# Performance work log

Measured on AMD Instinct MI355X. Metric: run time of the kernel, lower is better.

Reference implementation:

```python
import jax, jax.numpy as jnp
import numpy as np

DIM = 3072
HEADS = 24
HDIM = 128
MLP = 12288           # dim * mlp_ratio
B = 2
TEXT = 256
IMG = 1024
S = TEXT + IMG
TAU = 5.0
EPS = 1e-6


def setup_inputs() -> dict:
    key = jax.random.key(0)
    ks = jax.random.split(key, 16)
    w = lambda k, shape: jax.random.normal(k, shape, jnp.float32) * 0.02
    # rotary tables (cos/sin over pair dim HDIM//2)
    pos = jnp.arange(S, dtype=jnp.float32)
    inv_freq = 1.0 / (10000.0 ** (jnp.arange(0, HDIM, 2, dtype=jnp.float32) / HDIM))
    ang = pos[:, None] * inv_freq[None, :]            # [S, HDIM//2]
    return {
        "hidden_states": jax.random.normal(ks[0], (B, S, DIM), jnp.float32),
        "temb": jax.random.normal(ks[1], (B, DIM), jnp.float32),
        "rot_cos": jnp.cos(ang),
        "rot_sin": jnp.sin(ang),
        # AdaLayerNormZeroSingle: linear(silu(temb)) -> shift, scale, gate
        "w_ada": w(ks[2], (DIM, 3 * DIM)), "b_ada": jnp.zeros((3 * DIM,), jnp.float32),
        # attention qkv (bias=True) + rms_norm scales
        "wq": w(ks[3], (DIM, DIM)), "bq": jnp.zeros((DIM,), jnp.float32),
        "wk": w(ks[4], (DIM, DIM)), "bk": jnp.zeros((DIM,), jnp.float32),
        "wv": w(ks[5], (DIM, DIM)), "bv": jnp.zeros((DIM,), jnp.float32),
        "q_scale": jnp.ones((HDIM,), jnp.float32), "k_scale": jnp.ones((HDIM,), jnp.float32),
        # TokenSelect (conditioning proj + per-token score head)
        "w_cond": w(ks[6], (DIM, DIM)), "b_cond": jnp.zeros((DIM,), jnp.float32),
        "w_sel": w(ks[7], (DIM, 1)), "b_sel": jnp.zeros((1,), jnp.float32),
        # proj_mlp (DynaLinear, full width) and proj_out
        "w1": w(ks[8], (DIM, MLP)), "b1": jnp.zeros((MLP,), jnp.float32),
        "w2": w(ks[9], (DIM + MLP, DIM)), "b2": jnp.zeros((DIM,), jnp.float32),
        "text_len": TEXT,
        "img_len": IMG,
    }


def _forward(hidden_states, temb, rot_cos, rot_sin, w_ada, b_ada, wq, bq, wk, bk,
             wv, bv, q_scale, k_scale, w_cond, b_cond, w_sel, b_sel, w1, b1, w2, b2,
             text_len, img_len):
    Bn, Sn, C = hidden_states.shape
    residual = hidden_states

    # --- AdaLayerNormZeroSingle ---
    e = jax.nn.silu(temb) @ w_ada + b_ada
    shift, scale, gate = jnp.split(e, 3, axis=-1)          # each [B, C]
    mu = hidden_states.mean(-1, keepdims=True)
    var = hidden_states.var(-1, keepdims=True)
    x = (hidden_states - mu) * jax.lax.rsqrt(var + EPS)
    x = x * (1.0 + scale[:, None, :]) + shift[:, None, :]  # norm_hidden_states

    # --- self-attention (pre_only: no out proj), qk rms_norm, rope ---
    split_heads = lambda t: t.reshape(Bn, Sn, HEADS, HDIM)
    q = split_heads(x @ wq + bq)
    k = split_heads(x @ wk + bk)
    v = split_heads(x @ wv + bv)
    rmsn = lambda t, g: t * jax.lax.rsqrt(jnp.mean(t * t, -1, keepdims=True) + EPS) * g
    q = rmsn(q, q_scale)
    k = rmsn(k, k_scale)

    def rope(t):
        t1, t2 = t[..., 0::2], t[..., 1::2]
        c = rot_cos[None, :, None, :]
        s = rot_sin[None, :, None, :]
        r1 = t1 * c - t2 * s
        r2 = t1 * s + t2 * c
        return jnp.stack([r1, r2], axis=-1).reshape(t.shape)

    q, k = rope(q), rope(k)
    scores = jnp.einsum("bqhd,bkhd->bhqk", q, k) / np.float32(np.sqrt(HDIM))
    attn = jax.nn.softmax(scores, axis=-1)
    attn_out = jnp.einsum("bhqk,bkhd->bqhd", attn, v).reshape(Bn, Sn, C)

    # --- token selection on raw hidden states (img tokens, cond on temb + text) ---
    img_h = hidden_states[:, text_len:, :]
    text_h = hidden_states[:, :text_len, :]
    cond = jax.nn.silu(temb + text_h.mean(axis=1)) @ w_cond + b_cond   # [B, C]
    logits = (img_h + cond[:, None, :]) @ w_sel + b_sel                # [B, IMG, 1]
    soft = jax.nn.sigmoid(logits / TAU)
    hard = (soft > 0.5).astype(soft.dtype)
    mask = hard + soft - jax.lax.stop_gradient(soft)   # straight-through hard mask

    gelu = lambda t: jax.nn.gelu(t, approximate=True)

    # text branch: full-width dyna MLP
    text_mlp = gelu(x[:, :text_len] @ w1 + b1)
    text_out = jnp.concatenate([attn_out[:, :text_len], text_mlp], axis=-1) @ w2 + b2

    # img branch: gather/MLP/scatter is math-equivalent to masked dense compute
    # (unselected rows stay zero in the scatter buffer)
    img_mlp = gelu(x[:, text_len:] @ w1 + b1)
    img_out = (jnp.concatenate([attn_out[:, text_len:], img_mlp], axis=-1) @ w2 + b2) * mask

    out = jnp.concatenate([text_out, img_out], axis=1)
    return residual + gate[:, None, :] * out


def reference(hidden_states, temb, rot_cos, rot_sin, w_ada, b_ada, wq, bq, wk, bk,
              wv, bv, q_scale, k_scale, w_cond, b_cond, w_sel, b_sel, w1, b1, w2, b2,
              text_len, img_len):
    return _forward(hidden_states, temb, rot_cos, rot_sin, w_ada, b_ada, wq, bq, wk,
                    bk, wv, bv, q_scale, k_scale, w_cond, b_cond, w_sel, b_sel,
                    w1, b1, w2, b2, text_len, img_len)
```

## Files before the change

kernel.cpp:

```cpp
#include <hip/hip_runtime.h>
#include <hip/hip_bf16.h>


#define DIM    3072
#define NHEADS 24
#define HD     128
#define MLPD   12288
#define NB     2
#define TEXTL  256
#define IMGL   1024
#define SEQL   1280
#define NTOK   (NB*SEQL)
#define CATK   (DIM+MLPD)
#define EPSV   1e-6f

typedef unsigned short u16;
typedef __bf16 bf16x8 __attribute__((ext_vector_type(8)));
typedef float f32x4 __attribute__((ext_vector_type(4)));

__device__ __forceinline__ u16 f2bf(float f){
  unsigned u = __builtin_bit_cast(unsigned, f);
  u += 0x7fffu + ((u >> 16) & 1u);
  return (u16)(u >> 16);
}
__device__ __forceinline__ float siluf(float x){ return x / (1.f + __expf(-x)); }
__device__ __forceinline__ float geluf(float x){
  float t = 0.7978845608028654f * (x + 0.044715f * x * x * x);
  float th = 1.f - 2.f / (__expf(2.f * t) + 1.f);
  return 0.5f * x * (1.f + th);
}
__device__ __forceinline__ void ld_lds16(const void* g, void* l){
  __builtin_amdgcn_global_load_lds((const __attribute__((address_space(1))) void*)g,
                                   (__attribute__((address_space(3))) void*)l, 16, 0, 0);
}

__global__ __launch_bounds__(256)
void k_transpose_cvt(const float* __restrict__ W, u16* __restrict__ WT, int K, int N){
  __shared__ float tile[64][65];
  const int n0 = blockIdx.x * 64, k0 = blockIdx.y * 64;
  const int tx = threadIdx.x & 63, ty = threadIdx.x >> 6;
  #pragma unroll
  for (int i = 0; i < 16; ++i){
    const int r = ty + i*4;
    tile[r][tx] = W[(size_t)(k0 + r)*N + n0 + tx];
  }
  __syncthreads();
  #pragma unroll
  for (int i = 0; i < 16; ++i){
    const int r = ty + i*4;
    WT[(size_t)(n0 + r)*K + k0 + tx] = f2bf(tile[tx][r]);
  }
}

__global__ void k_cat3(const float* __restrict__ a, const float* __restrict__ b,
                       const float* __restrict__ c, float* __restrict__ o){
  const int i = blockIdx.x*256 + threadIdx.x;
  if (i < DIM) o[i] = a[i];
  else if (i < 2*DIM) o[i] = b[i - DIM];
  else o[i] = c[i - 2*DIM];
}

__global__ __launch_bounds__(256)
void k_ada(const float* __restrict__ temb, const float* __restrict__ w_ada,
           const float* __restrict__ b_ada, float* __restrict__ e){
  __shared__ float st[2*DIM];
  __shared__ float red[4][2][64];
  const int t = threadIdx.x;
  for (int i = t; i < 2*DIM; i += 256) st[i] = siluf(temb[i]);
  __syncthreads();
  const int tx = t & 63, ty = t >> 6;
  const int col = blockIdx.x*64 + tx;
  float a0 = 0.f, a1 = 0.f;
  for (int k = ty*768; k < ty*768 + 768; ++k){
    const float w = w_ada[(size_t)k*9216 + col];
    a0 += st[k]*w; a1 += st[DIM + k]*w;
  }
  red[ty][0][tx] = a0; red[ty][1][tx] = a1;
  __syncthreads();
  if (ty == 0){
    float s0 = red[0][0][tx] + red[1][0][tx] + red[2][0][tx] + red[3][0][tx];
    float s1 = red[0][1][tx] + red[1][1][tx] + red[2][1][tx] + red[3][1][tx];
    e[col]        = s0 + b_ada[col];
    e[9216 + col] = s1 + b_ada[col];
  }
}

__global__ void k_tmean(const float* __restrict__ h, float* __restrict__ tm){
  const int b = blockIdx.y;
  const int c = blockIdx.x*256 + threadIdx.x;
  float s = 0.f;
  for (int i = 0; i < TEXTL; ++i) s += h[((size_t)b*SEQL + i)*DIM + c];
  tm[b*DIM + c] = s * (1.f/TEXTL);
}

__global__ __launch_bounds__(256)
void k_cond(const float* __restrict__ temb, const float* __restrict__ tm,
            const float* __restrict__ w_cond, const float* __restrict__ b_cond,
            float* __restrict__ cond){
  __shared__ float st[2*DIM];
  __shared__ float red[4][2][64];
  const int t = threadIdx.x;
  for (int i = t; i < 2*DIM; i += 256) st[i] = siluf(temb[i] + tm[i]);
  __syncthreads();
  const int tx = t & 63, ty = t >> 6;
  const int col = blockIdx.x*64 + tx;
  float a0 = 0.f, a1 = 0.f;
  for (int k = ty*768; k < ty*768 + 768; ++k){
    const float w = w_cond[(size_t)k*DIM + col];
    a0 += st[k]*w; a1 += st[DIM + k]*w;
  }
  red[ty][0][tx] = a0; red[ty][1][tx] = a1;
  __syncthreads();
  if (ty == 0){
    float s0 = red[0][0][tx] + red[1][0][tx] + red[2][0][tx] + red[3][0][tx];
    float s1 = red[0][1][tx] + red[1][1][tx] + red[2][1][tx] + red[3][1][tx];
    cond[col]       = s0 + b_cond[col];
    cond[DIM + col] = s1 + b_cond[col];
  }
}

__global__ __launch_bounds__(256)
void k_sel(const float* __restrict__ h, const float* __restrict__ cond,
           const float* __restrict__ w_sel, const float* __restrict__ b_sel,
           float* __restrict__ maskb){
  const int lane = threadIdx.x & 63;
  const int wv = threadIdx.x >> 6;
  const int wid = blockIdx.x*4 + wv;
  const int b = wid >> 10, i = wid & 1023;
  const float* hr = h + ((size_t)b*SEQL + TEXTL + i)*DIM;
  const float* cr = cond + (size_t)b*DIM;
  float acc = 0.f;
  #pragma unroll
  for (int j = 0; j < 12; ++j){
    const int c4 = j*64 + lane;
    float4 hv = ((const float4*)hr)[c4];
    float4 cv = ((const float4*)cr)[c4];
    float4 wv4 = ((const float4*)w_sel)[c4];
    acc += (hv.x+cv.x)*wv4.x + (hv.y+cv.y)*wv4.y + (hv.z+cv.z)*wv4.z + (hv.w+cv.w)*wv4.w;
  }
  #pragma unroll
  for (int off = 1; off < 64; off <<= 1) acc += __shfl_xor(acc, off, 64);
  if (lane == 0) maskb[wid] = (acc + b_sel[0]) > 0.f ? 1.f : 0.f;
}

__global__ __launch_bounds__(256)
void k_lnmod(const float* __restrict__ h, const float* __restrict__ e,
             u16* __restrict__ xb){
  const int t = blockIdx.x;
  const int b = t / SEQL;
  const float* row = h + (size_t)t*DIM;
  float4 v[3];
  float s = 0.f, ss = 0.f;
  #pragma unroll
  for (int j = 0; j < 3; ++j){
    v[j] = ((const float4*)row)[threadIdx.x + j*256];
    s  += v[j].x + v[j].y + v[j].z + v[j].w;
    ss += v[j].x*v[j].x + v[j].y*v[j].y + v[j].z*v[j].z + v[j].w*v[j].w;
  }
  __shared__ float rs[4], rss[4];
  #pragma unroll
  for (int off = 1; off < 64; off <<= 1){
    s += __shfl_xor(s, off, 64); ss += __shfl_xor(ss, off, 64);
  }
  const int wv = threadIdx.x >> 6;
  if ((threadIdx.x & 63) == 0){ rs[wv] = s; rss[wv] = ss; }
  __syncthreads();
  s = rs[0]+rs[1]+rs[2]+rs[3]; ss = rss[0]+rss[1]+rss[2]+rss[3];
  const float mu = s * (1.f/DIM);
  const float var = ss * (1.f/DIM) - mu*mu;
  const float rstd = rsqrtf(var + EPSV);
  const float* sh = e + (size_t)b*9216;
  #pragma unroll
  for (int j = 0; j < 3; ++j){
    const int i4 = threadIdx.x + j*256;
    float4 sf = ((const float4*)sh)[i4];
    float4 sc = ((const float4*)(sh + DIM))[i4];
    ushort4 o;
    o.x = f2bf(((v[j].x - mu)*rstd)*(1.f + sc.x) + sf.x);
    o.y = f2bf(((v[j].y - mu)*rstd)*(1.f + sc.y) + sf.y);
    o.z = f2bf(((v[j].z - mu)*rstd)*(1.f + sc.z) + sf.z);
    o.w = f2bf(((v[j].w - mu)*rstd)*(1.f + sc.w) + sf.w);
    ((ushort4*)(xb + (size_t)t*DIM))[i4] = o;
  }
}

template<int MODE>
__global__ __launch_bounds__(256, 2)
void k_gemm(const u16* __restrict__ A, const u16* __restrict__ BT,
            const float* __restrict__ bias,
            float* __restrict__ Cf, u16* __restrict__ Cb,
            int K, int ldc, int col_off,
            size_t zsB, size_t zsC, size_t zsBias,
            const float* __restrict__ residual, const float* __restrict__ egate,
            const float* __restrict__ maskb){
  __shared__ __align__(16) u16 As[128*32];
  __shared__ __align__(16) u16 Bs[128*32];
  const int tid  = threadIdx.x;
  const int lane = tid & 63;
  const int wv   = tid >> 6;
  const int wr   = wv >> 1, wc = wv & 1;
  const int brow = blockIdx.y * 128, bcol = blockIdx.x * 128;
  const int l16 = lane & 15;
  const int g4  = lane >> 4;
  BT   += blockIdx.z * zsB;
  bias += blockIdx.z * zsBias;

  f32x4 acc[4][4] = {};
  const int nkt = K >> 5;
  for (int kt = 0; kt < nkt; ++kt){
    __syncthreads();
    #pragma unroll
    for (int c = 0; c < 2; ++c){
      const int Lb = wv*2048 + c*1024;
      const int row = (Lb + lane*16) >> 6;
      const int sch = (lane & 3) ^ ((row >> 1) & 3);
      ld_lds16(A + (size_t)(brow + row)*K + kt*32 + sch*8, (char*)As + Lb);
    }
    #pragma unroll
    for (int c = 0; c < 2; ++c){
      const int Lb = wv*2048 + c*1024;
      const int row = (Lb + lane*16) >> 6;
      const int sch = (lane & 3) ^ ((row >> 1) & 3);
      ld_lds16(BT + (size_t)(bcol + row)*K + kt*32 + sch*8, (char*)Bs + Lb);
    }
    __syncthreads();
    bf16x8 af[4], bfr[4];
    #pragma unroll
    for (int m = 0; m < 4; ++m){
      const int row = wr*64 + m*16 + l16;
      const int sch = g4 ^ ((row >> 1) & 3);
      af[m] = *(const bf16x8*)((const char*)As + row*64 + sch*16);
    }
    #pragma unroll
    for (int n = 0; n < 4; ++n){
      const int row = wc*64 + n*16 + l16;
      const int sch = g4 ^ ((row >> 1) & 3);
      bfr[n] = *(const bf16x8*)((const char*)Bs + row*64 + sch*16);
    }
    #pragma unroll
    for (int m = 0; m < 4; ++m)
      #pragma unroll
      for (int n = 0; n < 4; ++n)
        acc[m][n] = __builtin_amdgcn_mfma_f32_16x16x32_bf16(af[m], bfr[n], acc[m][n], 0, 0, 0);
  }
  float* Cfz = Cf + blockIdx.z * zsC;
  #pragma unroll
  for (int m = 0; m < 4; ++m){
    #pragma unroll
    for (int n = 0; n < 4; ++n){
      #pragma unroll
      for (int r = 0; r < 4; ++r){
        const int row = brow + wr*64 + m*16 + g4*4 + r;
        const int col = bcol + wc*64 + n*16 + l16;
        const float val = acc[m][n][r] + bias[col];
        if (MODE == 0){
          Cfz[(size_t)row*ldc + col] = val;
        } else if (MODE == 1){
          Cb[(size_t)row*ldc + col_off + col] = f2bf(geluf(val));
        } else {
          const int bb = row / SEQL;
          const int sidx = row - bb*SEQL;
          const float mk = (sidx < TEXTL) ? 1.f : maskb[bb*IMGL + sidx - TEXTL];
          Cfz[(size_t)row*ldc + col] = residual[(size_t)row*DIM + col]
                                     + egate[(size_t)bb*9216 + 2*DIM + col] * (val * mk);
        }
      }
    }
  }
}

__global__ __launch_bounds__(256)
void k_qkpost(const float* __restrict__ qkv, const float* __restrict__ rcos,
              const float* __restrict__ rsin, const float* __restrict__ qscale,
              const float* __restrict__ kscale, u16* __restrict__ qb,
              u16* __restrict__ kb){
  const int t = blockIdx.x;
  const int which = blockIdx.y;
  const float* src = qkv + ((size_t)which*NTOK + t)*DIM;
  const float* gvec = which == 0 ? qscale : kscale;
  u16* dst = which == 0 ? qb : kb;
  const int s = t % SEQL;
  const int lane = threadIdx.x & 63;
  const int wv = threadIdx.x >> 6;
  const int l32 = lane & 31;
  const int hh = lane >> 5;
  #pragma unroll
  for (int p = 0; p < 3; ++p){
    const int hidx = p*8 + wv*2 + hh;
    float4 v = ((const float4*)(src + hidx*HD))[l32];
    float ssq = v.x*v.x + v.y*v.y + v.z*v.z + v.w*v.w;
    #pragma unroll
    for (int off = 1; off < 32; off <<= 1) ssq += __shfl_xor(ssq, off, 64);
    const float rms = rsqrtf(ssq * (1.f/HD) + EPSV);
    const int d0 = l32*4;
    const float t0 = v.x*rms*gvec[d0],   t1 = v.y*rms*gvec[d0+1];
    const float t2 = v.z*rms*gvec[d0+2], t3 = v.w*rms*gvec[d0+3];
    const int i0 = l32*2;
    const float c0 = rcos[s*64 + i0],   s0 = rsin[s*64 + i0];
    const float c1 = rcos[s*64 + i0+1], s1 = rsin[s*64 + i0+1];
    ushort4 o;
    o.x = f2bf(t0*c0 - t1*s0);
    o.y = f2bf(t0*s0 + t1*c0);
    o.z = f2bf(t2*c1 - t3*s1);
    o.w = f2bf(t2*s1 + t3*c1);
    ((ushort4*)(dst + (size_t)t*DIM + hidx*HD))[l32] = o;
  }
}

__global__ __launch_bounds__(256)
void k_vpost(const float* __restrict__ qkv, u16* __restrict__ vt){
  __shared__ float tile[64][65];
  const int bh = blockIdx.x;
  const int st = blockIdx.y;
  const int dt = blockIdx.z;
  const int b = bh / NHEADS, hidx = bh % NHEADS;
  const float* v = qkv + (size_t)2*NTOK*DIM;
  const int tx = threadIdx.x & 63, ty = threadIdx.x >> 6;
  #pragma unroll
  for (int i = 0; i < 16; ++i){
    const int r = ty + i*4;
    tile[r][tx] = v[((size_t)b*SEQL + st*64 + r)*DIM + hidx*HD + dt*64 + tx];
  }
  __syncthreads();
  #pragma unroll
  for (int i = 0; i < 16; ++i){
    const int r = ty + i*4;
    vt[((size_t)bh*HD + dt*64 + r)*SEQL + st*64 + tx] = f2bf(tile[tx][r]);
  }
}

__global__ __launch_bounds__(256, 2)
void k_attn(const u16* __restrict__ q, const u16* __restrict__ kg,
            const u16* __restrict__ vt, u16* __restrict__ cat){
  __shared__ __align__(16) u16 Ks[64*128];
  __shared__ __align__(16) u16 Vs[128*64];
  __shared__ __align__(16) u16 Ps[4*16*64];
  const int lane = threadIdx.x & 63;
  const int wv = threadIdx.x >> 6;
  const int bh = blockIdx.y, b = bh / NHEADS, hidx = bh % NHEADS;
  const int qt = blockIdx.x;
  const int l16 = lane & 15;
  const int g4 = lane >> 4;

  bf16x8 qf[4];
  {
    const int qrow = qt*64 + wv*16 + l16;
    const u16* qptr = q + ((size_t)b*SEQL + qrow)*DIM + hidx*HD;
    #pragma unroll
    for (int ksi = 0; ksi < 4; ++ksi)
      qf[ksi] = *(const bf16x8*)(qptr + ksi*32 + g4*8);
  }
  f32x4 out[8] = {};
  float mreg[4] = {-1e30f, -1e30f, -1e30f, -1e30f};
  float lreg[4] = {0.f, 0.f, 0.f, 0.f};
  const float scl = 0.08838834764831845f;

  for (int kt = 0; kt < SEQL/64; ++kt){
    __syncthreads();
    #pragma unroll
    for (int c = 0; c < 4; ++c){
      const int Lb = wv*4096 + c*1024;
      const int row = (Lb + lane*16) >> 8;
      const int sch = (lane & 15) ^ (row & 7);
      ld_lds16(kg + ((size_t)b*SEQL + kt*64 + row)*DIM + hidx*HD + sch*8, (char*)Ks + Lb);
    }
    #pragma unroll
    for (int c = 0; c < 4; ++c){
      const int Lb = wv*4096 + c*1024;
      const int row = (Lb + lane*16) >> 7;
      const int sch = (lane & 7) ^ (row & 7);
      ld_lds16(vt + ((size_t)bh*HD + row)*SEQL + kt*64 + sch*8, (char*)Vs + Lb);
    }
    __syncthreads();
    f32x4 sf[4];
    #pragma unroll
    for (int kc = 0; kc < 4; ++kc){
      sf[kc] = (f32x4){0.f, 0.f, 0.f, 0.f};
      #pragma unroll
      for (int ksi = 0; ksi < 4; ++ksi){
        const int key = kc*16 + l16;
        const int c0 = ksi*4 + g4;
        const int sch = c0 ^ (key & 7);
        bf16x8 kbf = *(const bf16x8*)((const char*)Ks + key*256 + sch*16);
        sf[kc] = __builtin_amdgcn_mfma_f32_16x16x32_bf16(qf[ksi], kbf, sf[kc], 0, 0, 0);
      }
    }
    #pragma unroll
    for (int kc = 0; kc < 4; ++kc) sf[kc] *= scl;
    #pragma unroll
    for (int r = 0; r < 4; ++r){
      float mx = fmaxf(fmaxf(sf[0][r], sf[1][r]), fmaxf(sf[2][r], sf[3][r]));
      #pragma unroll
      for (int off = 1; off < 16; off <<= 1) mx = fmaxf(mx, __shfl_xor(mx, off, 64));
      const float mnew = fmaxf(mreg[r], mx);
      const float sfac = __expf(mreg[r] - mnew);
      mreg[r] = mnew;
      float rsum = 0.f;
      #pragma unroll
      for (int kc = 0; kc < 4; ++kc){
        const float p = __expf(sf[kc][r] - mnew);
        sf[kc][r] = p;
        rsum += p;
      }
      #pragma unroll
      for (int off = 1; off < 16; off <<= 1) rsum += __shfl_xor(rsum, off, 64);
      lreg[r] = lreg[r]*sfac + rsum;
      #pragma unroll
      for (int nc = 0; nc < 8; ++nc) out[nc][r] *= sfac;
    }
    #pragma unroll
    for (int kc = 0; kc < 4; ++kc){
      #pragma unroll
      for (int r = 0; r < 4; ++r){
        const int prow = g4*4 + r;
        int byte = prow*128 + (kc*16 + l16)*2;
        byte ^= (prow & 7) << 4;
        *(u16*)((char*)Ps + wv*2048 + byte) = f2bf(sf[kc][r]);
      }
    }
    __syncthreads();
    bf16x8 pa[2];
    #pragma unroll
    for (int k2 = 0; k2 < 2; ++k2){
      const int prow = l16;
      const int c0 = k2*4 + g4;
      const int sch = c0 ^ (prow & 7);
      pa[k2] = *(const bf16x8*)((const char*)Ps + wv*2048 + prow*128 + sch*16);
    }
    #pragma unroll
    for (int nc = 0; nc < 8; ++nc){
      #pragma unroll
      for (int k2 = 0; k2 < 2; ++k2){
        const int d = nc*16 + l16;
        const int c0 = k2*4 + g4;
        const int sch = c0 ^ (d & 7);
        bf16x8 vb = *(const bf16x8*)((const char*)Vs + d*128 + sch*16);
        out[nc] = __builtin_amdgcn_mfma_f32_16x16x32_bf16(pa[k2], vb, out[nc], 0, 0, 0);
      }
    }
  }
  #pragma unroll
  for (int nc = 0; nc < 8; ++nc){
    #pragma unroll
    for (int r = 0; r < 4; ++r){
      const int qrow = qt*64 + wv*16 + g4*4 + r;
      const int d = nc*16 + l16;
      cat[((size_t)b*SEQL + qrow)*CATK + hidx*HD + d] = f2bf(out[nc][r] / lreg[r]);
    }
  }
}

extern "C" void kernel_launch(void* const* d_in, const int* in_sizes, int n_in,
                              void* d_out, int out_size, void* d_ws, size_t ws_size,
                              hipStream_t stream){
  const float* hid    = (const float*)d_in[0];
  const float* temb   = (const float*)d_in[1];
  const float* rcos   = (const float*)d_in[2];
  const float* rsin   = (const float*)d_in[3];
  const float* w_ada  = (const float*)d_in[4];
  const float* b_ada  = (const float*)d_in[5];
  const float* wq     = (const float*)d_in[6];
  const float* bq     = (const float*)d_in[7];
  const float* wk     = (const float*)d_in[8];
  const float* bk     = (const float*)d_in[9];
  const float* wvw    = (const float*)d_in[10];
  const float* bv     = (const float*)d_in[11];
  const float* qs     = (const float*)d_in[12];
  const float* ksc    = (const float*)d_in[13];
  const float* w_cond = (const float*)d_in[14];
  const float* b_cond = (const float*)d_in[15];
  const float* w_sel  = (const float*)d_in[16];
  const float* b_sel  = (const float*)d_in[17];
  const float* w1     = (const float*)d_in[18];
  const float* b1     = (const float*)d_in[19];
  const float* w2     = (const float*)d_in[20];
  const float* b2     = (const float*)d_in[21];
  float* outp = (float*)d_out;

  char* ws = (char*)d_ws;
  u16* wT     = (u16*)ws;
  u16* xb     = wT + (size_t)DIM*CATK;
  float* qkvF = (float*)(xb + (size_t)NTOK*DIM);
  u16* cat    = (u16*)qkvF;
  u16* qb     = (u16*)(qkvF + (size_t)3*NTOK*DIM);
  u16* kbb    = qb + (size_t)NTOK*DIM;
  u16* vtb    = kbb + (size_t)NTOK*DIM;
  float* e    = (float*)(vtb + (size_t)NB*NHEADS*HD*SEQL);
  float* tm   = e + NB*9216;
  float* cond = tm + NB*DIM;
  float* maskb= cond + NB*DIM;
  float* bcat = maskb + NB*IMGL;

  dim3 blk(256);
  k_cat3<<<dim3(36), blk, 0, stream>>>(bq, bk, bv, bcat);
  k_ada<<<dim3(144), blk, 0, stream>>>(temb, w_ada, b_ada, e);
  k_tmean<<<dim3(12,2), blk, 0, stream>>>(hid, tm);
  k_cond<<<dim3(48), blk, 0, stream>>>(temb, tm, w_cond, b_cond, cond);
  k_sel<<<dim3(512), blk, 0, stream>>>(hid, cond, w_sel, b_sel, maskb);
  k_lnmod<<<dim3(NTOK), blk, 0, stream>>>(hid, e, xb);
  k_transpose_cvt<<<dim3(48,48),  blk, 0, stream>>>(wq,  wT,                     DIM, DIM);
  k_transpose_cvt<<<dim3(48,48),  blk, 0, stream>>>(wk,  wT + (size_t)DIM*DIM,   DIM, DIM);
  k_transpose_cvt<<<dim3(48,48),  blk, 0, stream>>>(wvw, wT + (size_t)2*DIM*DIM, DIM, DIM);
  k_gemm<0><<<dim3(24,20,3), blk, 0, stream>>>(xb, wT, bcat, qkvF, (u16*)nullptr,
      DIM, DIM, 0, (size_t)DIM*DIM, (size_t)NTOK*DIM, (size_t)DIM,
      nullptr, nullptr, nullptr);
  k_qkpost<<<dim3(NTOK,2), blk, 0, stream>>>(qkvF, rcos, rsin, qs, ksc, qb, kbb);
  k_vpost<<<dim3(48,20,2), blk, 0, stream>>>(qkvF, vtb);
  k_attn<<<dim3(20,48), blk, 0, stream>>>(qb, kbb, vtb, cat);
  k_transpose_cvt<<<dim3(192,48), blk, 0, stream>>>(w1, wT, DIM, MLPD);
  k_gemm<1><<<dim3(96,20), blk, 0, stream>>>(xb, wT, b1, (float*)nullptr, cat,
      DIM, CATK, DIM, 0, 0, 0, nullptr, nullptr, nullptr);
  k_transpose_cvt<<<dim3(48,240), blk, 0, stream>>>(w2, wT, CATK, DIM);
  k_gemm<2><<<dim3(24,20), blk, 0, stream>>>(cat, wT, b2, outp, (u16*)nullptr,
      CATK, DIM, 0, 0, 0, 0, hid, e, maskb);
}
```

Before: 1.700 ms.

## Split-K the proj_out GEMM with atomics and double-buffer LDS tiles

The final proj_out GEMM (K=15360) had only 480 blocks, so it now splits K four ways across blockIdx.z. Each split atomically adds its partial sums into a zeroed fp32 buffer, and a separate epilogue kernel then applies bias, mask, gate and residual. All GEMM modes also switch to double-buffered LDS staging, issuing the next tile's global-to-LDS load before computing on the current one and needing one barrier per iteration. The split adds a zero pass, atomic traffic and an extra elementwise kernel, and the extra LDS may lower occupancy.

```diff
diff --git a/kernel.cpp b/kernel.cpp
--- a/kernel.cpp
+++ b/kernel.cpp
@@ -13,6 +13,7 @@
 #define NTOK   (NB*SEQL)
 #define CATK   (DIM+MLPD)
 #define EPSV   1e-6f
+#define WSPLIT 4
 
 typedef unsigned short u16;
 typedef __bf16 bf16x8 __attribute__((ext_vector_type(8)));
@@ -58,6 +59,11 @@
   if (i < DIM) o[i] = a[i];
   else if (i < 2*DIM) o[i] = b[i - DIM];
   else o[i] = c[i - 2*DIM];
+}
+
+__global__ void k_zero(float* __restrict__ p, int n4){
+  const int i = blockIdx.x*256 + threadIdx.x;
+  if (i < n4) ((float4*)p)[i] = make_float4(0.f,0.f,0.f,0.f);
 }
 
 __global__ __launch_bounds__(256)
@@ -189,12 +195,12 @@
 void k_gemm(const u16* __restrict__ A, const u16* __restrict__ BT,
             const float* __restrict__ bias,
             float* __restrict__ Cf, u16* __restrict__ Cb,
-            int K, int ldc, int col_off,
+            int Kstride, int Kloop, int ldc, int col_off,
             size_t zsB, size_t zsC, size_t zsBias,
             const float* __restrict__ residual, const float* __restrict__ egate,
             const float* __restrict__ maskb){
-  __shared__ __align__(16) u16 As[128*32];
-  __shared__ __align__(16) u16 Bs[128*32];
+  __shared__ __align__(16) u16 As[2][128*32];
+  __shared__ __align__(16) u16 Bs[2][128*32];
   const int tid  = threadIdx.x;
   const int lane = tid & 63;
   const int wv   = tid >> 6;
@@ -202,48 +208,62 @@
   const int brow = blockIdx.y * 128, bcol = blockIdx.x * 128;
   const int l16 = lane & 15;
   const int g4  = lane >> 4;
-  BT   += blockIdx.z * zsB;
-  bias += blockIdx.z * zsBias;
-
-  f32x4 acc[4][4] = {};
-  const int nkt = K >> 5;
-  for (int kt = 0; kt < nkt; ++kt){
-    __syncthreads();
+  size_t koff = 0;
+  if (MODE == 3){
+    koff = (size_t)blockIdx.z * Kloop;
+  } else {
+    BT   += blockIdx.z * zsB;
+    bias += blockIdx.z * zsBias;
+  }
+  const u16* Ab = A  + koff;
+  const u16* Bb = BT + koff;
+
+  auto stage = [&](int buf, int kt){
     #pragma unroll
     for (int c = 0; c < 2; ++c){
       const int Lb = wv*2048 + c*1024;
       const int row = (Lb + lane*16) >> 6;
       const int sch = (lane & 3) ^ ((row >> 1) & 3);
-      ld_lds16(A + (size_t)(brow + row)*K + kt*32 + sch*8, (char*)As + Lb);
+      ld_lds16(Ab + (size_t)(brow + row)*Kstride + kt*32 + sch*8, (char*)As[buf] + Lb);
     }
     #pragma unroll
     for (int c = 0; c < 2; ++c){
       const int Lb = wv*2048 + c*1024;
       const int row = (Lb + lane*16) >> 6;
       const int sch = (lane & 3) ^ ((row >> 1) & 3);
-      ld_lds16(BT + (size_t)(bcol + row)*K + kt*32 + sch*8, (char*)Bs + Lb);
-    }
-    __syncthreads();
+      ld_lds16(Bb + (size_t)(bcol + row)*Kstride + kt*32 + sch*8, (char*)Bs[buf] + Lb);
+    }
+  };
+
+  f32x4 acc[4][4] = {};
+  const int nkt = Kloop >> 5;
+  stage(0, 0);
+  __syncthreads();
+  int buf = 0;
+  for (int kt = 0; kt < nkt; ++kt){
+    if (kt + 1 < nkt) stage(buf ^ 1, kt + 1);
     bf16x8 af[4], bfr[4];
     #pragma unroll
     for (int m = 0; m < 4; ++m){
       const int row = wr*64 + m*16 + l16;
       const int sch = g4 ^ ((row >> 1) & 3);
-      af[m] = *(const bf16x8*)((const char*)As + row*64 + sch*16);
+      af[m] = *(const bf16x8*)((const char*)As[buf] + row*64 + sch*16);
     }
     #pragma unroll
     for (int n = 0; n < 4; ++n){
       const int row = wc*64 + n*16 + l16;
       const int sch = g4 ^ ((row >> 1) & 3);
-      bfr[n] = *(const bf16x8*)((const char*)Bs + row*64 + sch*16);
+      bfr[n] = *(const bf16x8*)((const char*)Bs[buf] + row*64 + sch*16);
     }
     #pragma unroll
     for (int m = 0; m < 4; ++m)
       #pragma unroll
       for (int n = 0; n < 4; ++n)
         acc[m][n] = __builtin_amdgcn_mfma_f32_16x16x32_bf16(af[m], bfr[n], acc[m][n], 0, 0, 0);
-  }
-  float* Cfz = Cf + blockIdx.z * zsC;
+    __syncthreads();
+    buf ^= 1;
+  }
+  float* Cfz = (MODE == 3) ? Cf : (Cf + blockIdx.z * zsC);
   #pragma unroll
   for (int m = 0; m < 4; ++m){
     #pragma unroll
@@ -252,20 +272,50 @@
       for (int r = 0; r < 4; ++r){
         const int row = brow + wr*64 + m*16 + g4*4 + r;
         const int col = bcol + wc*64 + n*16 + l16;
-        const float val = acc[m][n][r] + bias[col];
-        if (MODE == 0){
-          Cfz[(size_t)row*ldc + col] = val;
-        } else if (MODE == 1){
-          Cb[(size_t)row*ldc + col_off + col] = f2bf(geluf(val));
+        if (MODE == 3){
+          atomicAdd(&Cfz[(size_t)row*ldc + col], acc[m][n][r]);
         } else {
-          const int bb = row / SEQL;
-          const int sidx = row - bb*SEQL;
-          const float mk = (sidx < TEXTL) ? 1.f : maskb[bb*IMGL + sidx - TEXTL];
-          Cfz[(size_t)row*ldc + col] = residual[(size_t)row*DIM + col]
-                                     + egate[(size_t)bb*9216 + 2*DIM + col] * (val * mk);
+          const float val = acc[m][n][r] + bias[col];
+          if (MODE == 0){
+            Cfz[(size_t)row*ldc + col] = val;
+          } else if (MODE == 1){
+            Cb[(size_t)row*ldc + col_off + col] = f2bf(geluf(val));
+          } else {
+            const int bb = row / SEQL;
+            const int sidx = row - bb*SEQL;
+            const float mk = (sidx < TEXTL) ? 1.f : maskb[bb*IMGL + sidx - TEXTL];
+            Cfz[(size_t)row*ldc + col] = residual[(size_t)row*DIM + col]
+                                       + egate[(size_t)bb*9216 + 2*DIM + col] * (val * mk);
+          }
         }
       }
     }
+  }
+}
+
+__global__ __launch_bounds__(256)
+void k_w2epi(const float* __restrict__ accum, const float* __restrict__ bias,
+             const float* __restrict__ residual, const float* __restrict__ egate,
+             const float* __restrict__ maskb, float* __restrict__ out){
+  const int row = blockIdx.x;
+  const int bb = row / SEQL, sidx = row - bb*SEQL;
+  const float mk = (sidx < TEXTL) ? 1.f : maskb[bb*IMGL + sidx - TEXTL];
+  const float* ar = accum + (size_t)row*DIM;
+  const float* rr = residual + (size_t)row*DIM;
+  const float* gr = egate + (size_t)bb*9216 + 2*DIM;
+  float* orow = out + (size_t)row*DIM;
+  #pragma unroll
+  for (int j = threadIdx.x; j < DIM/4; j += 256){
+    float4 a = ((const float4*)ar)[j];
+    float4 bv = ((const float4*)bias)[j];
+    float4 r = ((const float4*)rr)[j];
+    float4 g = ((const float4*)gr)[j];
+    float4 o;
+    o.x = r.x + g.x*((a.x + bv.x)*mk);
+    o.y = r.y + g.y*((a.y + bv.y)*mk);
+    o.z = r.z + g.z*((a.z + bv.z)*mk);
+    o.w = r.w + g.w*((a.w + bv.w)*mk);
+    ((float4*)orow)[j] = o;
   }
 }
 
@@ -485,6 +535,7 @@
   u16* qb     = (u16*)(qkvF + (size_t)3*NTOK*DIM);
   u16* kbb    = qb + (size_t)NTOK*DIM;
   u16* vtb    = kbb + (size_t)NTOK*DIM;
+  float* accum= (float*)qb;
   float* e    = (float*)(vtb + (size_t)NB*NHEADS*HD*SEQL);
   float* tm   = e + NB*9216;
   float* cond = tm + NB*DIM;
@@ -502,15 +553,17 @@
   k_transpose_cvt<<<dim3(48,48),  blk, 0, stream>>>(wk,  wT + (size_t)DIM*DIM,   DIM, DIM);
   k_transpose_cvt<<<dim3(48,48),  blk, 0, stream>>>(wvw, wT + (size_t)2*DIM*DIM, DIM, DIM);
   k_gemm<0><<<dim3(24,20,3), blk, 0, stream>>>(xb, wT, bcat, qkvF, (u16*)nullptr,
-      DIM, DIM, 0, (size_t)DIM*DIM, (size_t)NTOK*DIM, (size_t)DIM,
+      DIM, DIM, DIM, 0, (size_t)DIM*DIM, (size_t)NTOK*DIM, (size_t)DIM,
       nullptr, nullptr, nullptr);
   k_qkpost<<<dim3(NTOK,2), blk, 0, stream>>>(qkvF, rcos, rsin, qs, ksc, qb, kbb);
   k_vpost<<<dim3(48,20,2), blk, 0, stream>>>(qkvF, vtb);
   k_attn<<<dim3(20,48), blk, 0, stream>>>(qb, kbb, vtb, cat);
   k_transpose_cvt<<<dim3(192,48), blk, 0, stream>>>(w1, wT, DIM, MLPD);
   k_gemm<1><<<dim3(96,20), blk, 0, stream>>>(xb, wT, b1, (float*)nullptr, cat,
-      DIM, CATK, DIM, 0, 0, 0, nullptr, nullptr, nullptr);
+      DIM, DIM, CATK, DIM, 0, 0, 0, nullptr, nullptr, nullptr);
   k_transpose_cvt<<<dim3(48,240), blk, 0, stream>>>(w2, wT, CATK, DIM);
-  k_gemm<2><<<dim3(24,20), blk, 0, stream>>>(cat, wT, b2, outp, (u16*)nullptr,
-      CATK, DIM, 0, 0, 0, 0, hid, e, maskb);
-}
+  k_zero<<<dim3(NTOK*DIM/4/256), blk, 0, stream>>>(accum, NTOK*DIM/4);
+  k_gemm<3><<<dim3(24,20,WSPLIT), blk, 0, stream>>>(cat, wT, b2, accum, (u16*)nullptr,
+      CATK, CATK/WSPLIT, DIM, 0, 0, 0, 0, nullptr, nullptr, nullptr);
+  k_w2epi<<<dim3(NTOK), blk, 0, stream>>>(accum, b2, hid, e, maskb, outp);
+}
```

Measured after the change: 1.681 ms. Within noise of the previous version (-1.1%).
